# Kernel optimization log

Measured on AMD Instinct MI355X. Metric: run time of the kernel, lower is better.

The kernel has to match this reference:

```python
import jax, jax.numpy as jnp
import numpy as np

N_NODES = 100000
N_EDGES = 1600000
D_IN = 128
D_OUT = 128


def setup_inputs() -> dict:
    key = jax.random.key(0)
    k1, k2, k3, k4, k5 = jax.random.split(key, 5)
    x = jax.random.normal(k1, (N_NODES, D_IN), dtype=jnp.float32)
    edge_row = jax.random.randint(k2, (N_EDGES,), 0, N_NODES, dtype=jnp.int32)
    edge_col = jax.random.randint(k3, (N_EDGES,), 0, N_NODES, dtype=jnp.int32)
    edge_vals = jax.random.uniform(k4, (N_EDGES,), dtype=jnp.float32)
    stdv = 1.0 / np.sqrt(D_OUT)
    weight = jax.random.uniform(k5, (D_IN, D_OUT), dtype=jnp.float32,
                                minval=-stdv, maxval=stdv)
    return {"x": x, "edge_row": edge_row, "edge_col": edge_col,
            "edge_vals": edge_vals, "weight": weight}


def reference(x, edge_row, edge_col, edge_vals, weight):
    # spmm(adj, x): gather source features, scale by edge weight, segment-sum to dst
    n = x.shape[0]
    msgs = x[edge_col] * edge_vals[:, None]          # [E, D_IN]
    agg = jax.ops.segment_sum(msgs, edge_row, num_segments=n)  # [N, D_IN]
    # dense weight matmul
    return agg @ weight                               # [N, D_OUT]
```

## Files before the change

### kernel.cpp

```cpp
#include <hip/hip_runtime.h>
#include <hip/hip_fp16.h>


#define N_NODES 100000
#define N_EDGES 1600000
#define DIM     128
#define BROWS   32
#define CB      3125
#define NSUP    49
#define SLOTCAP1 34816
#define SLOTCAP2 640
#define CAP     1024
#define OCAP    2048
#define CPAD    16

#define EPB1   1024
#define PBLK1  ((N_EDGES + EPB1 - 1) / EPB1)
#define CHUNK2 1024
#define CPS    (SLOTCAP1 / CHUNK2)
#define PBLK2  (NSUP * CPS)

#define OFF_CCUR1  25600000
#define OFF_CCUR2  25604096
#define OFF_OCNT   25804096
#define OFF_OBUF   25804160
#define OFF_EBUF1  25836928
#define OFF_EBUF2  39484800

__global__ __launch_bounds__(256) void gemm_xw_kernel(
    const float* __restrict__ x,
    const float* __restrict__ W,
    __half*      __restrict__ y)
{
    __shared__ float As[32 * 32];
    __shared__ float Ws[32 * 128];

    const int t    = threadIdx.x;
    const int row0 = blockIdx.x * 32;
    const int r0   = (t >> 5) * 4;
    const int c0   = (t & 31) * 4;

    float acc[4][4];
#pragma unroll
    for (int i = 0; i < 4; ++i)
#pragma unroll
        for (int j = 0; j < 4; ++j) acc[i][j] = 0.f;

    for (int k0 = 0; k0 < 128; k0 += 32) {
        {
            int r  = t >> 3;
            int kp = t & 7;
            float4 a = *(const float4*)(x + (size_t)(row0 + r) * 128 + k0 + kp * 4);
            *(float4*)(As + r * 32 + kp * 4) = a;
        }
        {
            const float4* Wg = (const float4*)(W + (size_t)k0 * 128);
            float4* Wl = (float4*)Ws;
#pragma unroll
            for (int i = 0; i < 4; ++i) Wl[t + 256 * i] = Wg[t + 256 * i];
        }
        __syncthreads();

#pragma unroll
        for (int kk = 0; kk < 32; ++kk) {
            float4 w = *(const float4*)(Ws + kk * 128 + c0);
            float a0 = As[(r0 + 0) * 32 + kk];
            float a1 = As[(r0 + 1) * 32 + kk];
            float a2 = As[(r0 + 2) * 32 + kk];
            float a3 = As[(r0 + 3) * 32 + kk];
            acc[0][0] += a0 * w.x; acc[0][1] += a0 * w.y; acc[0][2] += a0 * w.z; acc[0][3] += a0 * w.w;
            acc[1][0] += a1 * w.x; acc[1][1] += a1 * w.y; acc[1][2] += a1 * w.z; acc[1][3] += a1 * w.w;
            acc[2][0] += a2 * w.x; acc[2][1] += a2 * w.y; acc[2][2] += a2 * w.z; acc[2][3] += a2 * w.w;
            acc[3][0] += a3 * w.x; acc[3][1] += a3 * w.y; acc[3][2] += a3 * w.z; acc[3][3] += a3 * w.w;
        }
        __syncthreads();
    }

#pragma unroll
    for (int i = 0; i < 4; ++i) {
        __half2 p0 = __floats2half2_rn(acc[i][0], acc[i][1]);
        __half2 p1 = __floats2half2_rn(acc[i][2], acc[i][3]);
        uint2 w;
        w.x = *(const unsigned*)&p0;
        w.y = *(const unsigned*)&p1;
        *(uint2*)(y + (size_t)(row0 + r0 + i) * 128 + c0) = w;
    }
}

__global__ __launch_bounds__(256) void zero_kernel(
    unsigned* ccur1, unsigned* ccur2, unsigned* ocnt)
{
    int i = blockIdx.x * 256 + threadIdx.x;
    if (i < NSUP) ccur1[i * CPAD] = 0u;
    if (i < CB)   ccur2[i * CPAD] = 0u;
    if (i == 0)   *ocnt = 0u;
}

__global__ __launch_bounds__(256) void partition1_kernel(
    const int*   __restrict__ erow,
    const int*   __restrict__ ecol,
    const float* __restrict__ eval,
    unsigned*    __restrict__ ccur1,
    unsigned*    __restrict__ ocnt,
    uint4*       __restrict__ obuf,
    uint2*       __restrict__ ebuf1)
{
    __shared__ unsigned hist[NSUP];
    __shared__ unsigned gbase[NSUP];
    const int t = threadIdx.x;
    const unsigned e0 = blockIdx.x * (unsigned)EPB1;

    if (t < NSUP) hist[t] = 0u;
    __syncthreads();

    unsigned r[4], c[4], v[4]; bool ok[4];
#pragma unroll
    for (int k = 0; k < 4; ++k) {
        unsigned e = e0 + (unsigned)k * 256u + t;
        ok[k] = (e < N_EDGES);
        unsigned es = ok[k] ? e : (N_EDGES - 1);
        r[k] = (unsigned)erow[es];
        c[k] = (unsigned)ecol[es];
        v[k] = __float_as_uint(eval[es]);
    }
#pragma unroll
    for (int k = 0; k < 4; ++k)
        if (ok[k]) atomicAdd(&hist[r[k] >> 11], 1u);
    __syncthreads();

    if (t < NSUP) {
        unsigned h = hist[t];
        gbase[t] = h ? atomicAdd(&ccur1[t * CPAD], h) : 0u;
        hist[t] = 0u;
    }
    __syncthreads();

#pragma unroll
    for (int k = 0; k < 4; ++k) {
        if (ok[k]) {
            unsigned s    = r[k] >> 11;
            unsigned rank = atomicAdd(&hist[s], 1u);
            unsigned slot = gbase[s] + rank;
            unsigned xw   = ((r[k] & 2047u) << 17) | c[k];
            if (slot < SLOTCAP1) {
                ebuf1[(size_t)s * SLOTCAP1 + slot] = make_uint2(xw, v[k]);
            } else {
                unsigned oi = atomicAdd(ocnt, 1u);
                if (oi < OCAP) obuf[oi] = make_uint4(xw, v[k], r[k] >> 5, 0u);
            }
        }
    }
}

__global__ __launch_bounds__(256) void partition2_kernel(
    const unsigned* __restrict__ ccur1,
    const uint2*    __restrict__ ebuf1,
    unsigned*       __restrict__ ccur2,
    unsigned*       __restrict__ ocnt,
    uint4*          __restrict__ obuf,
    uint2*          __restrict__ ebuf2)
{
    __shared__ unsigned hist[64];
    __shared__ unsigned gbase[64];
    const int t   = threadIdx.x;
    const int s   = blockIdx.x / CPS;
    const int ch  = blockIdx.x % CPS;

    unsigned cnt = ccur1[s * CPAD];
    if (cnt > SLOTCAP1) cnt = SLOTCAP1;
    const unsigned base = (unsigned)ch * CHUNK2;
    if (base >= cnt) return;
    const unsigned m = (cnt - base < CHUNK2) ? (cnt - base) : CHUNK2;

    if (t < 64) hist[t] = 0u;
    __syncthreads();

    uint2 rec[4]; bool ok[4];
#pragma unroll
    for (int k = 0; k < 4; ++k) {
        unsigned idx = (unsigned)k * 256u + t;
        ok[k] = (idx < m);
        rec[k] = ok[k] ? ebuf1[(size_t)s * SLOTCAP1 + base + idx] : make_uint2(0u, 0u);
    }
#pragma unroll
    for (int k = 0; k < 4; ++k)
        if (ok[k]) atomicAdd(&hist[(rec[k].x >> 22) & 63u], 1u);
    __syncthreads();

    if (t < 64) {
        unsigned h = hist[t];
        gbase[t] = h ? atomicAdd(&ccur2[(s * 64 + t) * CPAD], h) : 0u;
        hist[t] = 0u;
    }
    __syncthreads();

#pragma unroll
    for (int k = 0; k < 4; ++k) {
        if (ok[k]) {
            unsigned fin  = (rec[k].x >> 22) & 63u;
            unsigned rank = atomicAdd(&hist[fin], 1u);
            unsigned slot = gbase[fin] + rank;
            unsigned f    = (unsigned)s * 64u + fin;
            if (slot < SLOTCAP2) {
                ebuf2[(size_t)f * SLOTCAP2 + slot] = rec[k];
            } else {
                unsigned oi = atomicAdd(ocnt, 1u);
                if (oi < OCAP) obuf[oi] = make_uint4(rec[k].x, rec[k].y, f, 0u);
            }
        }
    }
}

__global__ __launch_bounds__(256) void bucket_agg_kernel(
    const __half*   __restrict__ y,
    const unsigned* __restrict__ ccur2,
    const unsigned* __restrict__ ocnt,
    const uint4*    __restrict__ obuf,
    const uint2*    __restrict__ ebuf2,
    float*          __restrict__ out)
{
    __shared__ uint2    raw[CAP];
    __shared__ uint2    sorted[CAP];
    __shared__ unsigned hist[BROWS];
    __shared__ unsigned sstart[BROWS];
    __shared__ unsigned scur[BROWS];
    __shared__ unsigned extn;

    const int t    = threadIdx.x;
    const int b    = blockIdx.x;
    const int lane = t & 63;
    const int wv   = t >> 6;

    const unsigned cnt = ccur2[b * CPAD];
    const unsigned n   = (cnt < SLOTCAP2) ? cnt : SLOTCAP2;
    const size_t   base = (size_t)b * SLOTCAP2;

    if (t == 0) extn = 0u;
    if (t < BROWS) hist[t] = 0u;
    __syncthreads();

    for (unsigned i = t; i < n; i += 256) {
        uint2 rec = ebuf2[base + i];
        raw[i] = rec;
        atomicAdd(&hist[(rec.x >> 17) & 31u], 1u);
    }

    unsigned oc = *ocnt;
    if (oc > OCAP) oc = OCAP;
    for (unsigned i = t; i < oc; i += 256) {
        uint4 o = obuf[i];
        if (o.z == (unsigned)b) {
            unsigned p = atomicAdd(&extn, 1u);
            if (n + p < CAP) {
                raw[n + p] = make_uint2(o.x, o.y);
                atomicAdd(&hist[(o.x >> 17) & 31u], 1u);
            }
        }
    }
    __syncthreads();

    unsigned m = n + extn;
    if (m > CAP) m = CAP;

    if (t < 64) {
        unsigned v = (t < BROWS) ? hist[t] : 0u;
        unsigned inc = v;
#pragma unroll
        for (int d = 1; d < 64; d <<= 1) {
            unsigned o = __shfl_up(inc, d);
            if (t >= d) inc += o;
        }
        unsigned excl = inc - v;
        if (t < BROWS) { sstart[t] = excl; scur[t] = excl; }
    }
    __syncthreads();

    for (unsigned i = t; i < m; i += 256) {
        uint2 rec = raw[i];
        unsigned p = atomicAdd(&scur[(rec.x >> 17) & 31u], 1u);
        sorted[p] = rec;
    }
    __syncthreads();

    for (int r = wv; r < BROWS; r += 4) {
        int row = b * BROWS + r;
        if (row >= N_NODES) break;
        float ax = 0.f, ay = 0.f;
        unsigned j = sstart[r], e = scur[r];
        for (; j + 4 <= e; j += 4) {
            uint2 r0 = sorted[j + 0];
            uint2 r1 = sorted[j + 1];
            uint2 r2 = sorted[j + 2];
            uint2 r3 = sorted[j + 3];
            const __half2 h0 = *((const __half2*)(y + (size_t)(r0.x & 0x1FFFFu) * 128) + lane);
            const __half2 h1 = *((const __half2*)(y + (size_t)(r1.x & 0x1FFFFu) * 128) + lane);
            const __half2 h2 = *((const __half2*)(y + (size_t)(r2.x & 0x1FFFFu) * 128) + lane);
            const __half2 h3 = *((const __half2*)(y + (size_t)(r3.x & 0x1FFFFu) * 128) + lane);
            float v0 = __uint_as_float(r0.y);
            float v1 = __uint_as_float(r1.y);
            float v2 = __uint_as_float(r2.y);
            float v3 = __uint_as_float(r3.y);
            float2 f0 = __half22float2(h0);
            float2 f1 = __half22float2(h1);
            float2 f2 = __half22float2(h2);
            float2 f3 = __half22float2(h3);
            ax = fmaf(f0.x, v0, ax); ay = fmaf(f0.y, v0, ay);
            ax = fmaf(f1.x, v1, ax); ay = fmaf(f1.y, v1, ay);
            ax = fmaf(f2.x, v2, ax); ay = fmaf(f2.y, v2, ay);
            ax = fmaf(f3.x, v3, ax); ay = fmaf(f3.y, v3, ay);
        }
        for (; j < e; ++j) {
            uint2 rr = sorted[j];
            const __half2 h = *((const __half2*)(y + (size_t)(rr.x & 0x1FFFFu) * 128) + lane);
            float v = __uint_as_float(rr.y);
            float2 f = __half22float2(h);
            ax = fmaf(f.x, v, ax); ay = fmaf(f.y, v, ay);
        }
        *((float2*)(out + (size_t)row * 128) + lane) = make_float2(ax, ay);
    }
}

extern "C" void kernel_launch(void* const* d_in, const int* in_sizes, int n_in,
                              void* d_out, int out_size, void* d_ws, size_t ws_size,
                              hipStream_t stream) {
    const float* x    = (const float*)d_in[0];
    const int*   erow = (const int*)d_in[1];
    const int*   ecol = (const int*)d_in[2];
    const float* eval = (const float*)d_in[3];
    const float* W    = (const float*)d_in[4];
    float* out = (float*)d_out;

    char* ws = (char*)d_ws;
    __half*   y     = (__half*)  (ws);
    unsigned* ccur1 = (unsigned*)(ws + OFF_CCUR1);
    unsigned* ccur2 = (unsigned*)(ws + OFF_CCUR2);
    unsigned* ocnt  = (unsigned*)(ws + OFF_OCNT);
    uint4*    obuf  = (uint4*)   (ws + OFF_OBUF);
    uint2*    ebuf1 = (uint2*)   (ws + OFF_EBUF1);
    uint2*    ebuf2 = (uint2*)   (ws + OFF_EBUF2);

    gemm_xw_kernel<<<N_NODES / 32, 256, 0, stream>>>(x, W, y);
    zero_kernel<<<(CB + 255) / 256, 256, 0, stream>>>(ccur1, ccur2, ocnt);
    partition1_kernel<<<PBLK1, 256, 0, stream>>>(erow, ecol, eval, ccur1, ocnt, obuf, ebuf1);
    partition2_kernel<<<PBLK2, 256, 0, stream>>>(ccur1, ebuf1, ccur2, ocnt, obuf, ebuf2);
    bucket_agg_kernel<<<CB, 256, 0, stream>>>(y, ccur2, ocnt, obuf, ebuf2, out);
}
```

Before: 262.8 us.

## Split first-pass partition counters into per-lane sub-buckets and transpose GEMM A tile

The first partition pass now spreads each super-bucket's global atomic counter and output region across 8 lanes selected by block index. This cuts contention on the 49 hot counters, and the second pass walks per-lane sub-buckets instead. Separately, the GEMM stores the x tile transposed and padded in shared memory, so each thread reads its 4 row values with one float4 load instead of four scalar loads. The change adds more second-pass blocks, many of which exit early, and a smaller per-lane capacity that could push more edges to the overflow path.

```diff
diff --git a/kernel.cpp b/kernel.cpp
--- a/kernel.cpp
+++ b/kernel.cpp
@@ -8,7 +8,9 @@
 #define BROWS   32
 #define CB      3125
 #define NSUP    49
-#define SLOTCAP1 34816
+#define LANES   8
+#define NLR     (NSUP * LANES)
+#define SLOT1   4608
 #define SLOTCAP2 640
 #define CAP     1024
 #define OCAP    2048
@@ -16,23 +18,23 @@
 
 #define EPB1   1024
 #define PBLK1  ((N_EDGES + EPB1 - 1) / EPB1)
-#define CHUNK2 1024
-#define CPS    (SLOTCAP1 / CHUNK2)
-#define PBLK2  (NSUP * CPS)
+#define CH2    1024
+#define CPL    ((SLOT1 + CH2 - 1) / CH2)
+#define PBLK2  (NLR * CPL)
 
 #define OFF_CCUR1  25600000
-#define OFF_CCUR2  25604096
-#define OFF_OCNT   25804096
-#define OFF_OBUF   25804160
-#define OFF_EBUF1  25836928
-#define OFF_EBUF2  39484800
+#define OFF_CCUR2  25625088
+#define OFF_OCNT   25825088
+#define OFF_OBUF   25825152
+#define OFF_EBUF1  25857920
+#define OFF_EBUF2  40308608
 
 __global__ __launch_bounds__(256) void gemm_xw_kernel(
     const float* __restrict__ x,
     const float* __restrict__ W,
     __half*      __restrict__ y)
 {
-    __shared__ float As[32 * 32];
+    __shared__ __align__(16) float AsT[32 * 36];
     __shared__ float Ws[32 * 128];
 
     const int t    = threadIdx.x;
@@ -51,7 +53,10 @@
             int r  = t >> 3;
             int kp = t & 7;
             float4 a = *(const float4*)(x + (size_t)(row0 + r) * 128 + k0 + kp * 4);
-            *(float4*)(As + r * 32 + kp * 4) = a;
+            AsT[(kp * 4 + 0) * 36 + r] = a.x;
+            AsT[(kp * 4 + 1) * 36 + r] = a.y;
+            AsT[(kp * 4 + 2) * 36 + r] = a.z;
+            AsT[(kp * 4 + 3) * 36 + r] = a.w;
         }
         {
             const float4* Wg = (const float4*)(W + (size_t)k0 * 128);
@@ -64,14 +69,11 @@
 #pragma unroll
         for (int kk = 0; kk < 32; ++kk) {
             float4 w = *(const float4*)(Ws + kk * 128 + c0);
-            float a0 = As[(r0 + 0) * 32 + kk];
-            float a1 = As[(r0 + 1) * 32 + kk];
-            float a2 = As[(r0 + 2) * 32 + kk];
-            float a3 = As[(r0 + 3) * 32 + kk];
-            acc[0][0] += a0 * w.x; acc[0][1] += a0 * w.y; acc[0][2] += a0 * w.z; acc[0][3] += a0 * w.w;
-            acc[1][0] += a1 * w.x; acc[1][1] += a1 * w.y; acc[1][2] += a1 * w.z; acc[1][3] += a1 * w.w;
-            acc[2][0] += a2 * w.x; acc[2][1] += a2 * w.y; acc[2][2] += a2 * w.z; acc[2][3] += a2 * w.w;
-            acc[3][0] += a3 * w.x; acc[3][1] += a3 * w.y; acc[3][2] += a3 * w.z; acc[3][3] += a3 * w.w;
+            float4 a = *(const float4*)(AsT + kk * 36 + r0);
+            acc[0][0] += a.x * w.x; acc[0][1] += a.x * w.y; acc[0][2] += a.x * w.z; acc[0][3] += a.x * w.w;
+            acc[1][0] += a.y * w.x; acc[1][1] += a.y * w.y; acc[1][2] += a.y * w.z; acc[1][3] += a.y * w.w;
+            acc[2][0] += a.z * w.x; acc[2][1] += a.z * w.y; acc[2][2] += a.z * w.z; acc[2][3] += a.z * w.w;
+            acc[3][0] += a.w * w.x; acc[3][1] += a.w * w.y; acc[3][2] += a.w * w.z; acc[3][3] += a.w * w.w;
         }
         __syncthreads();
     }
@@ -91,9 +93,9 @@
     unsigned* ccur1, unsigned* ccur2, unsigned* ocnt)
 {
     int i = blockIdx.x * 256 + threadIdx.x;
-    if (i < NSUP) ccur1[i * CPAD] = 0u;
-    if (i < CB)   ccur2[i * CPAD] = 0u;
-    if (i == 0)   *ocnt = 0u;
+    if (i < NLR) ccur1[i * CPAD] = 0u;
+    if (i < CB)  ccur2[i * CPAD] = 0u;
+    if (i == 0)  *ocnt = 0u;
 }
 
 __global__ __launch_bounds__(256) void partition1_kernel(
@@ -108,7 +110,8 @@
     __shared__ unsigned hist[NSUP];
     __shared__ unsigned gbase[NSUP];
     const int t = threadIdx.x;
-    const unsigned e0 = blockIdx.x * (unsigned)EPB1;
+    const unsigned e0   = blockIdx.x * (unsigned)EPB1;
+    const unsigned lane = blockIdx.x & (LANES - 1);
 
     if (t < NSUP) hist[t] = 0u;
     __syncthreads();
@@ -130,7 +133,7 @@
 
     if (t < NSUP) {
         unsigned h = hist[t];
-        gbase[t] = h ? atomicAdd(&ccur1[t * CPAD], h) : 0u;
+        gbase[t] = h ? atomicAdd(&ccur1[(t * LANES + lane) * CPAD], h) : 0u;
         hist[t] = 0u;
     }
     __syncthreads();
@@ -141,9 +144,10 @@
             unsigned s    = r[k] >> 11;
             unsigned rank = atomicAdd(&hist[s], 1u);
             unsigned slot = gbase[s] + rank;
+            unsigned q    = s * LANES + lane;
             unsigned xw   = ((r[k] & 2047u) << 17) | c[k];
-            if (slot < SLOTCAP1) {
-                ebuf1[(size_t)s * SLOTCAP1 + slot] = make_uint2(xw, v[k]);
+            if (slot < SLOT1) {
+                ebuf1[(size_t)q * SLOT1 + slot] = make_uint2(xw, v[k]);
             } else {
                 unsigned oi = atomicAdd(ocnt, 1u);
                 if (oi < OCAP) obuf[oi] = make_uint4(xw, v[k], r[k] >> 5, 0u);
@@ -162,15 +166,16 @@
 {
     __shared__ unsigned hist[64];
     __shared__ unsigned gbase[64];
-    const int t   = threadIdx.x;
-    const int s   = blockIdx.x / CPS;
-    const int ch  = blockIdx.x % CPS;
-
-    unsigned cnt = ccur1[s * CPAD];
-    if (cnt > SLOTCAP1) cnt = SLOTCAP1;
-    const unsigned base = (unsigned)ch * CHUNK2;
+    const int t  = threadIdx.x;
+    const int q  = blockIdx.x / CPL;
+    const int ch = blockIdx.x % CPL;
+    const int s  = q >> 3;
+
+    unsigned cnt = ccur1[q * CPAD];
+    if (cnt > SLOT1) cnt = SLOT1;
+    const unsigned base = (unsigned)ch * CH2;
     if (base >= cnt) return;
-    const unsigned m = (cnt - base < CHUNK2) ? (cnt - base) : CHUNK2;
+    const unsigned m = (cnt - base < CH2) ? (cnt - base) : CH2;
 
     if (t < 64) hist[t] = 0u;
     __syncthreads();
@@ -180,7 +185,7 @@
     for (int k = 0; k < 4; ++k) {
         unsigned idx = (unsigned)k * 256u + t;
         ok[k] = (idx < m);
-        rec[k] = ok[k] ? ebuf1[(size_t)s * SLOTCAP1 + base + idx] : make_uint2(0u, 0u);
+        rec[k] = ok[k] ? ebuf1[(size_t)q * SLOT1 + base + idx] : make_uint2(0u, 0u);
     }
 #pragma unroll
     for (int k = 0; k < 4; ++k)
```

New measurement: 235.9 us. 1.11x faster.
